# Optimization experiments

Measured on AMD Instinct MI355X. Metric: run time of the kernel, lower is better.

Reference implementation:

```python
import jax, jax.numpy as jnp
import numpy as np

K = 2            # num_classes (fixed in module)
THRESH = 0.01    # CdistThreshold
MAX_ITERS = 3    # loop breaks when Ci > 3 -> at most 3 work iterations


def _l2norm(x, eps=1e-12):
    # torch F.normalize(dim=1) on [N, C]-style rows -> normalize last axis here
    n = jnp.linalg.norm(x, axis=-1, keepdims=True)
    return x / jnp.maximum(n, eps)


def _step(feats, centers):
    """One k-means iteration, vectorized over batch.
    feats:   [B, N, C]  centers: [K, C]
    Returns (new_centers [K,C], CurDist scalar, labels [B,N])."""
    B = feats.shape[0]
    fn = _l2norm(feats)
    cn = _l2norm(centers)
    # cosine distance 0.5*(1 - cos_sim): [B, N, K]
    dists = 0.5 * (1.0 - jnp.einsum('bnc,kc->bnk', fn, cn))
    labels = jnp.argmin(dists, axis=-1)                      # [B, N]
    mask = jax.nn.one_hot(labels, K, dtype=feats.dtype)      # [B, N, K]
    sums = jnp.einsum('bnc,bnk->bkc', feats, mask)           # [B, K, C]
    counts = jnp.sum(mask, axis=1)                           # [B, K]
    centers_iter = sums / (counts[..., None] + 1.0)          # [B, K, C] (note +1 as in torch)
    # per-batch mean cosine similarity between new per-batch centers and old centers
    num = jnp.sum(centers_iter * centers[None], axis=-1)     # [B, K]
    den = jnp.maximum(
        jnp.linalg.norm(centers_iter, axis=-1) * jnp.linalg.norm(centers, axis=-1)[None],
        1e-8)
    cdist = jnp.mean(num / den, axis=-1)                     # [B]
    new_centers = jnp.sum(centers_iter, axis=0) / B          # centersIterout / B
    cur_dist = jnp.sum(cdist) / B                            # CdistT / B
    return new_centers, cur_dist, labels


def setup_inputs() -> dict:
    key = jax.random.key(0)
    k1, k2 = jax.random.split(key)
    FeatureT = jax.random.normal(k1, (8, 256, 256, 256), dtype=jnp.float32)
    centerInit = jax.random.normal(k2, (K, 256), dtype=jnp.float32)
    return {"FeatureT": FeatureT, "centerInit": centerInit}


def reference(FeatureT, centerInit):
    B, C = FeatureT.shape[0], FeatureT.shape[1]
    feats = FeatureT.reshape(B, C, -1).transpose(0, 2, 1)    # [B, N, C]
    # iteration 1 always runs (centers = centerInit)
    centers, cur_dist, labels = _step(feats, centerInit)
    done = cur_dist < THRESH
    # iterations 2..3, frozen once converged (matches the while-loop break)
    for _ in range(MAX_ITERS - 1):
        nc, cd, lb = _step(feats, centers)
        centers = jnp.where(done, centers, nc)
        labels = jnp.where(done, labels, lb)
        cur_dist = jnp.where(done, cur_dist, cd)
        done = done | (cur_dist < THRESH)
    labels_onehot = jax.nn.one_hot(labels.reshape(-1), K, dtype=jnp.float32)  # [B*N, K]
    # torch returns centersIterout.detach()
    return jax.lax.stop_gradient(centers), labels, labels_onehot, cur_dist
```

## Files before the change

kernel.cpp:

```cpp
#include <hip/hip_runtime.h>
#include <stdint.h>

#define CDIM   256
#define NPIX   65536
#define NBATCH 8
#define WCOLS  64
#define NTILES 1024
#define TPB    16
#define NBLOCKS (NBATCH * NTILES / TPB)
#define KTHRESH 0.01

#define WS_DELTA 0
#define WS_CENT  256
#define WS_T     768
#define WS_S1    2816
#define WS_CNT   4864
#define WS_DONE  4872

#define OUT_LABELS 512
#define OUT_ONEHOT (512 + NBATCH * NPIX)
#define OUT_CDIST  (512 + NBATCH * NPIX + 2 * NBATCH * NPIX)

#define TILE_WORDS 16664

__device__ __forceinline__ void dma_row4(const float* g, float* l) {
  __builtin_amdgcn_global_load_lds((const __attribute__((address_space(1))) void*)g,
                                   (__attribute__((address_space(3))) void*)l, 4, 0, 0);
}

__device__ __forceinline__ double block_reduce(double v, double* sh) {
  const int t = threadIdx.x;
  #pragma unroll
  for (int off = 32; off > 0; off >>= 1) v += __shfl_down(v, off, 64);
  __syncthreads();
  if ((t & 63) == 0) sh[t >> 6] = v;
  __syncthreads();
  return sh[0] + sh[1] + sh[2] + sh[3];
}

__device__ __forceinline__ void block_reduce4(double v[4], double* sh) {
  const int t = threadIdx.x;
  #pragma unroll
  for (int off = 32; off > 0; off >>= 1) {
    v[0] += __shfl_down(v[0], off, 64);
    v[1] += __shfl_down(v[1], off, 64);
    v[2] += __shfl_down(v[2], off, 64);
    v[3] += __shfl_down(v[3], off, 64);
  }
  __syncthreads();
  if ((t & 63) == 0) {
    const int w = t >> 6;
    sh[w] = v[0]; sh[4 + w] = v[1]; sh[8 + w] = v[2]; sh[12 + w] = v[3];
  }
  __syncthreads();
  #pragma unroll
  for (int k = 0; k < 4; ++k) v[k] = sh[4 * k] + sh[4 * k + 1] + sh[4 * k + 2] + sh[4 * k + 3];
}

__global__ __launch_bounds__(256) void init_kernel(const float* __restrict__ cinit,
                                                   float* __restrict__ ws) {
  __shared__ double sh[16];
  const int t = threadIdx.x;
  for (int i = t; i < NBATCH * CDIM; i += 256) { ws[WS_T + i] = 0.f; ws[WS_S1 + i] = 0.f; }
  if (t < NBATCH) ((unsigned int*)(ws + WS_CNT))[t] = 0u;
  if (t == 0) ((int*)(ws + WS_DONE))[0] = 0;
  const float c0f = cinit[t], c1f = cinit[CDIM + t];
  ws[WS_CENT + t] = c0f;
  ws[WS_CENT + CDIM + t] = c1f;
  const double c0 = (double)c0f, c1 = (double)c1f;
  double n0 = sqrt(block_reduce(c0 * c0, sh));
  double n1 = sqrt(block_reduce(c1 * c1, sh));
  n0 = fmax(n0, 1e-12); n1 = fmax(n1, 1e-12);
  ws[WS_DELTA + t] = (float)(c1 / n1) - (float)(c0 / n0);
}

__global__ __launch_bounds__(256, 1) void pass_kernel(const float* __restrict__ F,
                                                      float* __restrict__ ws,
                                                      float* __restrict__ out,
                                                      int iter) {
  if (iter > 0 && ((const volatile int*)(ws + WS_DONE))[0] != 0) return;

  __shared__ float tile[2][TILE_WORDS];
  __shared__ float deltaS[4 * 72];

  const int t  = threadIdx.x;
  const int w  = t >> 6;
  const int l  = t & 63;
  const int b  = blockIdx.x >> 6;
  const int tile0 = (blockIdx.x & 63) * TPB;

  if (t < CDIM) deltaS[(t >> 6) * 72 + (t & 63)] = ws[WS_DELTA + t];

  const float* Fb = F + (size_t)b * CDIM * NPIX;

  {
    const size_t g0 = (size_t)(tile0 * WCOLS) + l;
    #pragma unroll
    for (int r = 0; r < 64; ++r) {
      const int c = w * 64 + r;
      dma_row4(Fb + (size_t)c * NPIX + g0, &tile[0][65 * c + 8 * (c >> 6) + l]);
    }
  }

  float s1[4] = {0.f, 0.f, 0.f, 0.f};
  float tv[4] = {0.f, 0.f, 0.f, 0.f};
  unsigned cnt = 0;

  const int cseg = l >> 4;
  const int q    = l & 15;
  const int nloc = w * 16 + q;

  int buf = 0;
  for (int i = 0; i < TPB; ++i) {
    asm volatile("s_waitcnt vmcnt(0)" ::: "memory");
    __syncthreads();

    if (i + 1 < TPB) {
      const size_t g0 = (size_t)((tile0 + i + 1) * WCOLS) + l;
      float* dst = tile[buf ^ 1];
      #pragma unroll
      for (int r = 0; r < 64; ++r) {
        const int c = w * 64 + r;
        dma_row4(Fb + (size_t)c * NPIX + g0, &dst[65 * c + 8 * (c >> 6) + l]);
      }
    }

    const float* T = tile[buf];

    double d = 0.0;
    const float* Tcol = T + (size_t)(cseg * 64) * 65 + 8 * cseg + nloc;
    const float* dl = deltaS + cseg * 72;
    #pragma unroll
    for (int j = 0; j < 64; ++j)
      d = fma((double)dl[j], (double)Tcol[(size_t)j * 65], d);
    d += __shfl_down(d, 32, 64);
    d += __shfl_down(d, 16, 64);
    const unsigned long long ball = __ballot(d > 0.0);
    const unsigned mask16 = (unsigned)(ball & 0xFFFFull);
    cnt += __popc(mask16);

    const int n0 = (tile0 + i) * WCOLS;
    if (l < 16) {
      const float m = (float)((mask16 >> l) & 1u);
      const int gi = b * NPIX + n0 + w * 16 + l;
      out[OUT_LABELS + gi] = m;
      ((float2*)(out + OUT_ONEHOT))[gi] = make_float2(1.0f - m, m);
    }

    #pragma unroll
    for (int k = 0; k < 4; ++k) {
      const float* row = T + (size_t)(l + 64 * k) * 65 + 8 * k + w * 16;
      float a1 = 0.f, at = 0.f;
      #pragma unroll
      for (int qq = 0; qq < 16; ++qq) {
        const float v = row[qq];
        a1 = fmaf((float)((mask16 >> qq) & 1u), v, a1);
        at += v;
      }
      s1[k] += a1;
      tv[k] += at;
    }
    buf ^= 1;
  }

  #pragma unroll
  for (int k = 0; k < 4; ++k) {
    unsafeAtomicAdd(&ws[WS_S1 + b * CDIM + l + 64 * k], s1[k]);
    if (iter == 0) unsafeAtomicAdd(&ws[WS_T + b * CDIM + l + 64 * k], tv[k]);
  }
  if (l == 0) atomicAdd(&((unsigned int*)(ws + WS_CNT))[b], cnt);
}

__global__ __launch_bounds__(256) void finalize_kernel(float* __restrict__ ws,
                                                       float* __restrict__ out) {
  __shared__ double sh[16];
  const int t = threadIdx.x;
  if (((const volatile int*)(ws + WS_DONE))[0] != 0) return;

  const double cold0 = (double)ws[WS_CENT + t];
  const double cold1 = (double)ws[WS_CENT + CDIM + t];
  const double normc0 = sqrt(block_reduce(cold0 * cold0, sh));
  const double normc1 = sqrt(block_reduce(cold1 * cold1, sh));

  double acc0 = 0.0, acc1 = 0.0, cdsum = 0.0;
  for (int b = 0; b < NBATCH; ++b) {
    const double s1v  = (double)ws[WS_S1 + b * CDIM + t];
    const double totv = (double)ws[WS_T  + b * CDIM + t];
    const double c1n  = (double)((unsigned int*)(ws + WS_CNT))[b];
    const double ci1  = s1v / (c1n + 1.0);
    const double ci0  = (totv - s1v) / ((double)NPIX - c1n + 1.0);
    acc0 += ci0; acc1 += ci1;
    double v[4] = {ci0 * cold0, ci0 * ci0, ci1 * cold1, ci1 * ci1};
    block_reduce4(v, sh);
    const double den0 = fmax(sqrt(v[1]) * normc0, 1e-8);
    const double den1 = fmax(sqrt(v[3]) * normc1, 1e-8);
    cdsum += 0.5 * (v[0] / den0 + v[2] / den1);
  }
  const double curdist = cdsum / (double)NBATCH;
  const float nc0f = (float)(acc0 / (double)NBATCH);
  const float nc1f = (float)(acc1 / (double)NBATCH);

  ws[WS_CENT + t] = nc0f;
  ws[WS_CENT + CDIM + t] = nc1f;
  out[t] = nc0f;
  out[CDIM + t] = nc1f;
  if (t == 0) out[OUT_CDIST] = (float)curdist;

  double m0 = sqrt(block_reduce((double)nc0f * (double)nc0f, sh));
  double m1 = sqrt(block_reduce((double)nc1f * (double)nc1f, sh));
  m0 = fmax(m0, 1e-12); m1 = fmax(m1, 1e-12);
  ws[WS_DELTA + t] = (float)((double)nc1f / m1) - (float)((double)nc0f / m0);

  __syncthreads();
  for (int i = t; i < NBATCH * CDIM; i += 256) ws[WS_S1 + i] = 0.f;
  if (t < NBATCH) ((unsigned int*)(ws + WS_CNT))[t] = 0u;
  if (t == 0) ((int*)(ws + WS_DONE))[0] = (curdist < KTHRESH) ? 1 : 0;
}

extern "C" void kernel_launch(void* const* d_in, const int* in_sizes, int n_in,
                              void* d_out, int out_size, void* d_ws, size_t ws_size,
                              hipStream_t stream) {
  const float* F     = (const float*)d_in[0];
  const float* cinit = (const float*)d_in[1];
  float* out = (float*)d_out;
  float* ws  = (float*)d_ws;

  init_kernel<<<1, 256, 0, stream>>>(cinit, ws);
  for (int iter = 0; iter < 3; ++iter) {
    pass_kernel<<<NBLOCKS, 256, 0, stream>>>(F, ws, out, iter);
    finalize_kernel<<<1, 256, 0, stream>>>(ws, out);
  }
}
```

Baseline: 1.137 ms.

## Replace LDS-tiled pass with two-sweep register streaming over 1024-column slabs

```diff
diff --git a/kernel.cpp b/kernel.cpp
--- a/kernel.cpp
+++ b/kernel.cpp
@@ -4,10 +4,9 @@
 #define CDIM   256
 #define NPIX   65536
 #define NBATCH 8
-#define WCOLS  64
-#define NTILES 1024
-#define TPB    16
-#define NBLOCKS (NBATCH * NTILES / TPB)
+#define SLABS  64
+#define SCOLS  1024
+#define NBLOCKS (NBATCH * SLABS)
 #define KTHRESH 0.01
 
 #define WS_DELTA 0
@@ -20,13 +19,6 @@
 #define OUT_LABELS 512
 #define OUT_ONEHOT (512 + NBATCH * NPIX)
 #define OUT_CDIST  (512 + NBATCH * NPIX + 2 * NBATCH * NPIX)
-
-#define TILE_WORDS 16664
-
-__device__ __forceinline__ void dma_row4(const float* g, float* l) {
-  __builtin_amdgcn_global_load_lds((const __attribute__((address_space(1))) void*)g,
-                                   (__attribute__((address_space(3))) void*)l, 4, 0, 0);
-}
 
 __device__ __forceinline__ double block_reduce(double v, double* sh) {
   const int t = threadIdx.x;
@@ -74,101 +66,87 @@
   ws[WS_DELTA + t] = (float)(c1 / n1) - (float)(c0 / n0);
 }
 
-__global__ __launch_bounds__(256, 1) void pass_kernel(const float* __restrict__ F,
-                                                      float* __restrict__ ws,
-                                                      float* __restrict__ out,
-                                                      int iter) {
+__global__ __launch_bounds__(256) void pass_kernel(const float* __restrict__ F,
+                                                   float* __restrict__ ws,
+                                                   float* __restrict__ out,
+                                                   int iter) {
   if (iter > 0 && ((const volatile int*)(ws + WS_DONE))[0] != 0) return;
 
-  __shared__ float tile[2][TILE_WORDS];
-  __shared__ float deltaS[4 * 72];
-
-  const int t  = threadIdx.x;
-  const int w  = t >> 6;
-  const int l  = t & 63;
-  const int b  = blockIdx.x >> 6;
-  const int tile0 = (blockIdx.x & 63) * TPB;
-
-  if (t < CDIM) deltaS[(t >> 6) * 72 + (t & 63)] = ws[WS_DELTA + t];
-
-  const float* Fb = F + (size_t)b * CDIM * NPIX;
+  __shared__ double deltaD[CDIM];
+  __shared__ float s1p[CDIM * 4];
+  __shared__ float tp[CDIM * 4];
+  __shared__ unsigned cntS;
+
+  const int t = threadIdx.x;
+  const int w = t >> 6;
+  const int l = t & 63;
+  const int b = blockIdx.x >> 6;
+  const int n0 = (blockIdx.x & 63) * SCOLS;
+
+  if (t < CDIM) deltaD[t] = (double)ws[WS_DELTA + t];
+  if (t == 0) cntS = 0u;
+  __syncthreads();
+
+  const float4* __restrict__ Fv =
+      (const float4*)(F + (size_t)b * CDIM * NPIX + n0);
+  const int rstride = NPIX / 4;
+
+  double d0 = 0.0, d1 = 0.0, d2 = 0.0, d3 = 0.0;
+  #pragma unroll 16
+  for (int c = 0; c < CDIM; ++c) {
+    const float4 v = Fv[(size_t)c * rstride + t];
+    const double dc = deltaD[c];
+    d0 = fma(dc, (double)v.x, d0);
+    d1 = fma(dc, (double)v.y, d1);
+    d2 = fma(dc, (double)v.z, d2);
+    d3 = fma(dc, (double)v.w, d3);
+  }
+  const float m0 = d0 > 0.0 ? 1.f : 0.f;
+  const float m1 = d1 > 0.0 ? 1.f : 0.f;
+  const float m2 = d2 > 0.0 ? 1.f : 0.f;
+  const float m3 = d3 > 0.0 ? 1.f : 0.f;
+
+  const int gi0 = b * NPIX + n0 + 4 * t;
+  *(float4*)(out + OUT_LABELS + gi0) = make_float4(m0, m1, m2, m3);
+  *(float4*)(out + OUT_ONEHOT + 2 * gi0)     = make_float4(1.f - m0, m0, 1.f - m1, m1);
+  *(float4*)(out + OUT_ONEHOT + 2 * gi0 + 4) = make_float4(1.f - m2, m2, 1.f - m3, m3);
+
+  const unsigned cw = (unsigned)(__popcll(__ballot(d0 > 0.0)) +
+                                 __popcll(__ballot(d1 > 0.0)) +
+                                 __popcll(__ballot(d2 > 0.0)) +
+                                 __popcll(__ballot(d3 > 0.0)));
+  if (l == 0) atomicAdd(&cntS, cw);
+
+  const bool first = (iter == 0);
+  #pragma unroll 8
+  for (int c = CDIM - 1; c >= 0; --c) {
+    const float4 v = Fv[(size_t)c * rstride + t];
+    float s1 = 0.f;
+    s1 = fmaf(m0, v.x, s1);
+    s1 = fmaf(m1, v.y, s1);
+    s1 = fmaf(m2, v.z, s1);
+    s1 = fmaf(m3, v.w, s1);
+    #pragma unroll
+    for (int off = 32; off > 0; off >>= 1) s1 += __shfl_down(s1, off, 64);
+    if (l == 0) s1p[4 * c + w] = s1;
+    if (first) {
+      float tc = (v.x + v.y) + (v.z + v.w);
+      #pragma unroll
+      for (int off = 32; off > 0; off >>= 1) tc += __shfl_down(tc, off, 64);
+      if (l == 0) tp[4 * c + w] = tc;
+    }
+  }
+  __syncthreads();
 
   {
-    const size_t g0 = (size_t)(tile0 * WCOLS) + l;
-    #pragma unroll
-    for (int r = 0; r < 64; ++r) {
-      const int c = w * 64 + r;
-      dma_row4(Fb + (size_t)c * NPIX + g0, &tile[0][65 * c + 8 * (c >> 6) + l]);
+    const float s = (s1p[4 * t] + s1p[4 * t + 1]) + (s1p[4 * t + 2] + s1p[4 * t + 3]);
+    unsafeAtomicAdd(&ws[WS_S1 + b * CDIM + t], s);
+    if (first) {
+      const float tt = (tp[4 * t] + tp[4 * t + 1]) + (tp[4 * t + 2] + tp[4 * t + 3]);
+      unsafeAtomicAdd(&ws[WS_T + b * CDIM + t], tt);
     }
   }
-
-  float s1[4] = {0.f, 0.f, 0.f, 0.f};
-  float tv[4] = {0.f, 0.f, 0.f, 0.f};
-  unsigned cnt = 0;
-
-  const int cseg = l >> 4;
-  const int q    = l & 15;
-  const int nloc = w * 16 + q;
-
-  int buf = 0;
-  for (int i = 0; i < TPB; ++i) {
-    asm volatile("s_waitcnt vmcnt(0)" ::: "memory");
-    __syncthreads();
-
-    if (i + 1 < TPB) {
-      const size_t g0 = (size_t)((tile0 + i + 1) * WCOLS) + l;
-      float* dst = tile[buf ^ 1];
-      #pragma unroll
-      for (int r = 0; r < 64; ++r) {
-        const int c = w * 64 + r;
-        dma_row4(Fb + (size_t)c * NPIX + g0, &dst[65 * c + 8 * (c >> 6) + l]);
-      }
-    }
-
-    const float* T = tile[buf];
-
-    double d = 0.0;
-    const float* Tcol = T + (size_t)(cseg * 64) * 65 + 8 * cseg + nloc;
-    const float* dl = deltaS + cseg * 72;
-    #pragma unroll
-    for (int j = 0; j < 64; ++j)
-      d = fma((double)dl[j], (double)Tcol[(size_t)j * 65], d);
-    d += __shfl_down(d, 32, 64);
-    d += __shfl_down(d, 16, 64);
-    const unsigned long long ball = __ballot(d > 0.0);
-    const unsigned mask16 = (unsigned)(ball & 0xFFFFull);
-    cnt += __popc(mask16);
-
-    const int n0 = (tile0 + i) * WCOLS;
-    if (l < 16) {
-      const float m = (float)((mask16 >> l) & 1u);
-      const int gi = b * NPIX + n0 + w * 16 + l;
-      out[OUT_LABELS + gi] = m;
-      ((float2*)(out + OUT_ONEHOT))[gi] = make_float2(1.0f - m, m);
-    }
-
-    #pragma unroll
-    for (int k = 0; k < 4; ++k) {
-      const float* row = T + (size_t)(l + 64 * k) * 65 + 8 * k + w * 16;
-      float a1 = 0.f, at = 0.f;
-      #pragma unroll
-      for (int qq = 0; qq < 16; ++qq) {
-        const float v = row[qq];
-        a1 = fmaf((float)((mask16 >> qq) & 1u), v, a1);
-        at += v;
-      }
-      s1[k] += a1;
-      tv[k] += at;
-    }
-    buf ^= 1;
-  }
-
-  #pragma unroll
-  for (int k = 0; k < 4; ++k) {
-    unsafeAtomicAdd(&ws[WS_S1 + b * CDIM + l + 64 * k], s1[k]);
-    if (iter == 0) unsafeAtomicAdd(&ws[WS_T + b * CDIM + l + 64 * k], tv[k]);
-  }
-  if (l == 0) atomicAdd(&((unsigned int*)(ws + WS_CNT))[b], cnt);
+  if (t == 0) atomicAdd(&((unsigned int*)(ws + WS_CNT))[b], cntS);
 }
 
 __global__ __launch_bounds__(256) void finalize_kernel(float* __restrict__ ws,
```

Result: slower. 1.396 ms (+22.7%).
